# Kernel optimization log

Hardware: AMD Instinct MI355X
Metric: run time of the kernel (lower is better)

The kernel has to match this reference:

```python
import jax, jax.numpy as jnp
import numpy as np

N = 100000
E = 3200000
F_IN = 128
HID = 16
C = 8


def setup_inputs() -> dict:
    key = jax.random.key(0)
    k1, k2, k3, k4 = jax.random.split(key, 4)
    x = jax.random.normal(k1, (N, F_IN), dtype=jnp.float32)
    edge_index = jax.random.randint(k2, (2, E), 0, N, dtype=jnp.int64)
    W1 = jax.random.normal(k3, (F_IN, HID), dtype=jnp.float32) * (1.0 / np.sqrt(F_IN))
    b1 = jnp.zeros((HID,), dtype=jnp.float32)
    W2 = jax.random.normal(k4, (HID, C), dtype=jnp.float32) * (1.0 / np.sqrt(HID))
    b2 = jnp.zeros((C,), dtype=jnp.float32)
    return {"x": x, "edge_index": edge_index, "W1": W1, "b1": b1, "W2": W2, "b2": b2, "num_nodes": N}


def gcn_conv(x, src, dst, norm, W, b, num_nodes):
    # x: [N, F_in], src/dst: [E+N] (self-loops appended), norm: [E+N]
    h = x @ W                                # dense transform first (small out dim)
    msg = h[src] * norm[:, None]             # gather + edgewise scale
    out = jax.ops.segment_sum(msg, dst, num_segments=num_nodes)  # scatter-add
    return out + b


def reference(x, edge_index, W1, b1, W2, b2, num_nodes):
    # GCN normalization with self-loops: D^-1/2 (A+I) D^-1/2
    loop = jnp.arange(num_nodes, dtype=edge_index.dtype)
    src = jnp.concatenate([edge_index[0], loop])
    dst = jnp.concatenate([edge_index[1], loop])
    deg = jax.ops.segment_sum(jnp.ones_like(dst, dtype=x.dtype), dst, num_segments=num_nodes)
    dinv = jnp.where(deg > 0, jax.lax.rsqrt(deg), 0.0)
    norm = dinv[src] * dinv[dst]             # [E+N]

    h = jax.nn.relu(gcn_conv(x, src, dst, norm, W1, b1, num_nodes))
    # Dropout(p=0.5) in eval mode -> identity
    logits = gcn_conv(h, src, dst, norm, W2, b2, num_nodes)
    return jax.nn.log_softmax(logits, axis=1)
```

## Files before the change

### kernel.cpp

```cpp
#include <hip/hip_runtime.h>
#include <hip/hip_fp16.h>
#include <math.h>

#define FIN 128
#define HID 16
#define NC 8
#define BSH 8
#define BUKN 256
#define MAXBUK 512
#define CAP 10240
#define EPT 8
#define ACH (512 * EPT)

__device__ __forceinline__ __half2 shfl2(__half2 v, int m) {
    unsigned u = *(unsigned*)&v;
    u = __shfl_xor(u, m, 64);
    return *(__half2*)&u;
}

__global__ __launch_bounds__(512) void passA_kernel(
        const void* __restrict__ ei, int E, int N,
        int* __restrict__ pcur, unsigned* __restrict__ pakbuf, int nbuk) {
    const long long* p64 = (const long long*)ei;
    int ok = 1;
#pragma unroll
    for (int i = 0; i < 16; ++i) {
        long long v = p64[i];
        if (v < 0 || v >= (long long)N) ok = 0;
    }
    const int is64 = ok;
    const int* __restrict__ e32 = (const int*)ei;
    const int vecOK = is64 ? ((E & 1) == 0) : ((E & 3) == 0);
    __shared__ int cnt[MAXBUK], scn[MAXBUK], sbase[MAXBUK];
    __shared__ unsigned spv[ACH];
    __shared__ unsigned short sbk[ACH];
    const int t = threadIdx.x;
    for (long long c0 = (long long)blockIdx.x * ACH; c0 < E;
         c0 += (long long)gridDim.x * ACH) {
        cnt[t] = 0;
        __syncthreads();
        const long long e0 = c0 + (long long)t * EPT;
        const bool full = vecOK && (e0 + EPT <= E);
        int bv[EPT], rk[EPT];
        unsigned pv[EPT];
        if (full) {
            int ds[EPT], ss[EPT];
            if (is64) {
                const int4* pd = (const int4*)(e32 + 2 * ((long long)E + e0));
                const int4* ps = (const int4*)(e32 + 2 * e0);
                int4 a = pd[0], b = pd[1], c = pd[2], d = pd[3];
                ds[0]=a.x; ds[1]=a.z; ds[2]=b.x; ds[3]=b.z;
                ds[4]=c.x; ds[5]=c.z; ds[6]=d.x; ds[7]=d.z;
                int4 e = ps[0], f = ps[1], g = ps[2], h = ps[3];
                ss[0]=e.x; ss[1]=e.z; ss[2]=f.x; ss[3]=f.z;
                ss[4]=g.x; ss[5]=g.z; ss[6]=h.x; ss[7]=h.z;
            } else {
                const int4* pd = (const int4*)(e32 + (long long)E + e0);
                const int4* ps = (const int4*)(e32 + e0);
                int4 a = pd[0], b = pd[1];
                ds[0]=a.x; ds[1]=a.y; ds[2]=a.z; ds[3]=a.w;
                ds[4]=b.x; ds[5]=b.y; ds[6]=b.z; ds[7]=b.w;
                int4 e = ps[0], f = ps[1];
                ss[0]=e.x; ss[1]=e.y; ss[2]=e.z; ss[3]=e.w;
                ss[4]=f.x; ss[5]=f.y; ss[6]=f.z; ss[7]=f.w;
            }
#pragma unroll
            for (int i = 0; i < EPT; ++i) {
                int dd = ds[i];
                bv[i] = dd >> BSH;
                pv[i] = (unsigned)ss[i] | ((unsigned)(dd & (BUKN - 1)) << 24);
                rk[i] = atomicAdd(&cnt[bv[i]], 1);
            }
        } else {
#pragma unroll
            for (int i = 0; i < EPT; ++i) {
                long long e = e0 + i;
                bv[i] = -1;
                if (e < E) {
                    int dd = e32[is64 ? 2 * ((long long)E + e) : ((long long)E + e)];
                    int ssc = e32[is64 ? 2 * e : e];
                    bv[i] = dd >> BSH;
                    pv[i] = (unsigned)ssc | ((unsigned)(dd & (BUKN - 1)) << 24);
                    rk[i] = atomicAdd(&cnt[bv[i]], 1);
                }
            }
        }
        __syncthreads();
        int v = cnt[t];
        scn[t] = v;
        __syncthreads();
        for (int d = 1; d < MAXBUK; d <<= 1) {
            int add = (t >= d) ? scn[t - d] : 0;
            __syncthreads();
            scn[t] += add;
            __syncthreads();
        }
        int excl = scn[t] - v;
        __syncthreads();
        scn[t] = excl;
        if (t < nbuk) sbase[t] = v ? atomicAdd(&pcur[t * 16], v) : 0;
        __syncthreads();
#pragma unroll
        for (int i = 0; i < EPT; ++i) {
            if (bv[i] >= 0) {
                int s = scn[bv[i]] + rk[i];
                spv[s] = pv[i];
                sbk[s] = (unsigned short)bv[i];
            }
        }
        __syncthreads();
        int total = (int)((E - c0 < ACH) ? (E - c0) : ACH);
        for (int s = t; s < total; s += 512) {
            int b = sbk[s];
            int rel = sbase[b] + (s - scn[b]);
            if (rel < CAP) pakbuf[b * CAP + rel] = spv[s];
        }
        __syncthreads();
    }
}

__global__ __launch_bounds__(512) void passC2_kernel(
        const unsigned* __restrict__ pak, const int* __restrict__ pcur,
        int* __restrict__ csr_src, int* __restrict__ off,
        float* __restrict__ dinv, int N) {
    __shared__ int c[BUKN], sc[BUKN], cur[BUKN];
    const int b = blockIdx.x, t = threadIdx.x;
    if (t < BUKN) c[t] = 0;
    __syncthreads();
    const int ebeg = b * CAP;
    int cntb = pcur[b * 16];
    if (cntb > CAP) cntb = CAP;
    const int eend = ebeg + cntb;
    for (int i = ebeg + t; i < eend; i += 512)
        atomicAdd(&c[pak[i] >> 24], 1);
    __syncthreads();
    int v = (t < BUKN) ? c[t] : 0;
    if (t < BUKN) sc[t] = v;
    __syncthreads();
    for (int d = 1; d < 256; d <<= 1) {
        int add = (t < BUKN && t >= d) ? sc[t - d] : 0;
        __syncthreads();
        if (t < BUKN) sc[t] += add;
        __syncthreads();
    }
    if (t < BUKN) cur[t] = ebeg + sc[t] - v;
    __syncthreads();
    for (int i = ebeg + t; i < eend; i += 512) {
        unsigned w = pak[i];
        int pos = atomicAdd(&cur[w >> 24], 1);
        csr_src[pos] = (int)(w & 0xFFFFFFu);
    }
    __syncthreads();
    int n = (b << BSH) + t;
    if (t < BUKN && n < N) {
        off[n] = cur[t];
        dinv[n] = rsqrtf((float)(v + 1));
    }
}

__global__ void transform1_kernel(const float* __restrict__ x,
                                  const float* __restrict__ W1,
                                  const float* __restrict__ dinv,
                                  __half* __restrict__ g1, int N) {
    __shared__ float xs[16][FIN + 4];
    __shared__ float w[FIN][HID];
    const int t = threadIdx.x;
    for (int i = t; i < FIN * HID; i += 256) w[i / HID][i % HID] = W1[i];

    const float4* x4 = (const float4*)x;
    for (int rb = blockIdx.x * 16; rb < N; rb += gridDim.x * 16) {
        __syncthreads();
        for (int i = t; i < 16 * FIN / 4; i += 256) {
            int r = i >> 5, f4 = i & 31;
            int row = rb + r;
            float4 v = (row < N) ? x4[(size_t)row * (FIN / 4) + f4]
                                 : make_float4(0.f, 0.f, 0.f, 0.f);
            *((float4*)&xs[r][f4 * 4]) = v;
        }
        __syncthreads();
        int r = t >> 4, k = t & 15;
        int row = rb + r;
        if (row < N) {
            float s = 0.f;
#pragma unroll
            for (int f = 0; f < FIN; ++f) s += xs[r][f] * w[f][k];
            g1[(size_t)row * HID + k] = __float2half(s * dinv[row]);
        }
    }
}

__global__ void agg1_kernel(const int* __restrict__ off, const int* __restrict__ csr_src,
                            const __half2* __restrict__ g1h, const float* __restrict__ dinv,
                            const float* __restrict__ b1, const float* __restrict__ W2,
                            float4* __restrict__ g2q_out, int N) {
    const float4* g1q = (const float4*)g1h;
    __shared__ float w2s[HID][NC];
    for (int i = threadIdx.x; i < HID * NC; i += blockDim.x)
        w2s[i >> 3][i & 7] = W2[i];
    __syncthreads();
    int wid = threadIdx.x >> 6;
    int lane = threadIdx.x & 63;
    int sub = lane >> 4;
    int r = lane & 15;
    int hi = r & 1;
    int j = r >> 1;
    float4 bA = ((const float4*)b1)[hi * 2];
    float4 bB = ((const float4*)b1)[hi * 2 + 1];
    int wavesTotal = gridDim.x * (blockDim.x >> 6);
    for (int base = (blockIdx.x * (blockDim.x >> 6) + wid) * 4; base < N;
         base += wavesTotal * 4) {
        int n = base + sub;
        bool act = n < N;
        int start = 0, end = 0;
        float4 selfraw;
        if (act) {
            start = (n & (BUKN - 1)) ? off[n - 1] : (n >> BSH) * CAP;
            end = off[n];
            if (r < 2) selfraw = g1q[(size_t)n * 2 + hi];
        }
        __half2 a0 = __float2half2_rn(0.f), a1 = a0, a2 = a0, a3 = a0;
        for (int e = start + j; e < end; e += 8) {
            float4 raw = g1q[(size_t)csr_src[e] * 2 + hi];
            const __half2* rh = (const __half2*)&raw;
            a0 = __hadd2(a0, rh[0]); a1 = __hadd2(a1, rh[1]);
            a2 = __hadd2(a2, rh[2]); a3 = __hadd2(a3, rh[3]);
        }
#pragma unroll
        for (int m = 2; m <= 8; m <<= 1) {
            a0 = __hadd2(a0, shfl2(a0, m)); a1 = __hadd2(a1, shfl2(a1, m));
            a2 = __hadd2(a2, shfl2(a2, m)); a3 = __hadd2(a3, shfl2(a3, m));
        }
        if (act && r < 2) {
            float di = dinv[n];
            float2 s01 = __half22float2(a0), s23 = __half22float2(a1);
            float2 s45 = __half22float2(a2), s67 = __half22float2(a3);
            float2 f0 = __half22float2(*(__half2*)&selfraw.x);
            float2 f1 = __half22float2(*(__half2*)&selfraw.y);
            float2 f2 = __half22float2(*(__half2*)&selfraw.z);
            float2 f3 = __half22float2(*(__half2*)&selfraw.w);
            float h8[8];
            h8[0] = fmaxf(di * (s01.x + f0.x) + bA.x, 0.f);
            h8[1] = fmaxf(di * (s01.y + f0.y) + bA.y, 0.f);
            h8[2] = fmaxf(di * (s23.x + f1.x) + bA.z, 0.f);
            h8[3] = fmaxf(di * (s23.y + f1.y) + bA.w, 0.f);
            h8[4] = fmaxf(di * (s45.x + f2.x) + bB.x, 0.f);
            h8[5] = fmaxf(di * (s45.y + f2.y) + bB.y, 0.f);
            h8[6] = fmaxf(di * (s67.x + f3.x) + bB.z, 0.f);
            h8[7] = fmaxf(di * (s67.y + f3.y) + bB.w, 0.f);
            float part[8];
#pragma unroll
            for (int c = 0; c < 8; ++c) {
                float acc = 0.f;
#pragma unroll
                for (int k = 0; k < 8; ++k) acc += h8[k] * w2s[hi * 8 + k][c];
                part[c] = acc;
            }
#pragma unroll
            for (int c = 0; c < 8; ++c) part[c] += __shfl_xor(part[c], 1, 64);
            if (r == 0) {
                __half2 p0 = __floats2half2_rn(part[0] * di, part[1] * di);
                __half2 p1 = __floats2half2_rn(part[2] * di, part[3] * di);
                __half2 p2 = __floats2half2_rn(part[4] * di, part[5] * di);
                __half2 p3 = __floats2half2_rn(part[6] * di, part[7] * di);
                float4 o;
                *(__half2*)&o.x = p0; *(__half2*)&o.y = p1;
                *(__half2*)&o.z = p2; *(__half2*)&o.w = p3;
                g2q_out[n] = o;
            }
        }
    }
}

__global__ void agg2_kernel(const int* __restrict__ off, const int* __restrict__ csr_src,
                            const __half2* __restrict__ g2h, const float* __restrict__ dinv,
                            const float* __restrict__ b2, float* __restrict__ out, int N) {
    const float4* g2q = (const float4*)g2h;
    int wid = threadIdx.x >> 6;
    int lane = threadIdx.x & 63;
    int sub = lane >> 3, sl = lane & 7;
    float4 b2A = ((const float4*)b2)[0];
    float4 b2B = ((const float4*)b2)[1];
    int wavesTotal = gridDim.x * (blockDim.x >> 6);
    for (int base = (blockIdx.x * (blockDim.x >> 6) + wid) * 8; base < N;
         base += wavesTotal * 8) {
        int n = base + sub;
        bool act = n < N;
        int start = 0, end = 0;
        float4 selfraw;
        if (act) {
            start = (n & (BUKN - 1)) ? off[n - 1] : (n >> BSH) * CAP;
            end = off[n];
            selfraw = g2q[n];
        }
        __half2 a0 = __float2half2_rn(0.f), a1 = a0, a2 = a0, a3 = a0;
        for (int e = start + sl; e < end; e += 8) {
            float4 raw = g2q[csr_src[e]];
            const __half2* rh = (const __half2*)&raw;
            a0 = __hadd2(a0, rh[0]); a1 = __hadd2(a1, rh[1]);
            a2 = __hadd2(a2, rh[2]); a3 = __hadd2(a3, rh[3]);
        }
#pragma unroll
        for (int m = 1; m <= 4; m <<= 1) {
            a0 = __hadd2(a0, shfl2(a0, m)); a1 = __hadd2(a1, shfl2(a1, m));
            a2 = __hadd2(a2, shfl2(a2, m)); a3 = __hadd2(a3, shfl2(a3, m));
        }
        if (act) {
            float di = dinv[n];
            float2 s01 = __half22float2(a0), s23 = __half22float2(a1);
            float2 s45 = __half22float2(a2), s67 = __half22float2(a3);
            float2 f0 = __half22float2(*(__half2*)&selfraw.x);
            float2 f1 = __half22float2(*(__half2*)&selfraw.y);
            float2 f2 = __half22float2(*(__half2*)&selfraw.z);
            float2 f3 = __half22float2(*(__half2*)&selfraw.w);
            float l0 = di * (s01.x + f0.x) + b2A.x;
            float l1 = di * (s01.y + f0.y) + b2A.y;
            float l2 = di * (s23.x + f1.x) + b2A.z;
            float l3 = di * (s23.y + f1.y) + b2A.w;
            float l4 = di * (s45.x + f2.x) + b2B.x;
            float l5 = di * (s45.y + f2.y) + b2B.y;
            float l6 = di * (s67.x + f3.x) + b2B.z;
            float l7 = di * (s67.y + f3.y) + b2B.w;
            float m0 = fmaxf(fmaxf(fmaxf(l0, l1), fmaxf(l2, l3)),
                             fmaxf(fmaxf(l4, l5), fmaxf(l6, l7)));
            float se = __expf(l0 - m0) + __expf(l1 - m0) + __expf(l2 - m0) +
                       __expf(l3 - m0) + __expf(l4 - m0) + __expf(l5 - m0) +
                       __expf(l6 - m0) + __expf(l7 - m0);
            float lse = m0 + __logf(se);
            if (sl < 2) {
                float4 o;
                if (sl == 0) { o.x=l0-lse; o.y=l1-lse; o.z=l2-lse; o.w=l3-lse; }
                else         { o.x=l4-lse; o.y=l5-lse; o.z=l6-lse; o.w=l7-lse; }
                ((float4*)&out[(size_t)n * NC])[sl] = o;
            }
        }
    }
}

extern "C" void kernel_launch(void* const* d_in, const int* in_sizes, int n_in,
                              void* d_out, int out_size, void* d_ws, size_t ws_size,
                              hipStream_t stream) {
    const float* x  = (const float*)d_in[0];
    const void*  ei = d_in[1];
    const float* W1 = (const float*)d_in[2];
    const float* b1 = (const float*)d_in[3];
    const float* W2 = (const float*)d_in[4];
    const float* b2 = (const float*)d_in[5];

    const int N = in_sizes[0] / FIN;
    const int E = in_sizes[1] / 2;
    const int nbuk = (N + BUKN - 1) >> BSH;

    char* p = (char*)d_ws;
    unsigned* pakbuf = (unsigned*)p;     p += (size_t)nbuk * CAP * 4;
    int*    csr_src = (int*)p;           p += (size_t)nbuk * CAP * 4;
    __half* g1h     = (__half*)p;        p += (size_t)N * HID * 2;
    __half* g2h     = (__half*)p;        p += (size_t)N * NC * 2;
    int*    off     = (int*)p;           p += (size_t)N * 4;
    float*  dinv    = (float*)p;         p += (size_t)N * 4;
    int*    pcur    = (int*)p;           p += (size_t)MAXBUK * 16 * 4;

    hipMemsetAsync(pcur, 0, (size_t)MAXBUK * 16 * 4, stream);
    passA_kernel<<<(E + ACH - 1) / ACH, 512, 0, stream>>>(ei, E, N, pcur,
                                                          pakbuf, nbuk);
    passC2_kernel<<<nbuk, 512, 0, stream>>>(pakbuf, pcur, csr_src, off, dinv, N);

    int t1grid = (N + 15) / 16; if (t1grid > 2048) t1grid = 2048;
    transform1_kernel<<<t1grid, 256, 0, stream>>>(x, W1, dinv, g1h, N);
    agg1_kernel<<<(N + 15) / 16, 256, 0, stream>>>(off, csr_src, (const __half2*)g1h,
                                                   dinv, b1, W2, (float4*)g2h, N);
    agg2_kernel<<<(N + 31) / 32, 256, 0, stream>>>(off, csr_src, (const __half2*)g2h,
                                                   dinv, b2, (float*)d_out, N);
}
```

Measured before the change: 135.4 us.

## Stage bucket edges in LDS and unroll gather loops for more loads in flight

In the CSR build kernel, each bucket's packed edges are now copied into LDS during the counting pass and read back from LDS in the placement pass, so the second global read of the bucket is avoided. The two aggregation kernels now unroll the neighbour gather loop by two with separate accumulators, keeping two independent index/feature loads in flight per lane. The dense transform splits its dot product into four partial sums to break the serial FMA chain. The LDS staging adds 40KB of shared memory per block, which may reduce occupancy, and the extra accumulators raise register use.

After: 132.2 us. 1.02x faster.

```diff
diff --git a/kernel.cpp b/kernel.cpp
--- a/kernel.cpp
+++ b/kernel.cpp
@@ -124,15 +124,18 @@
         int* __restrict__ csr_src, int* __restrict__ off,
         float* __restrict__ dinv, int N) {
     __shared__ int c[BUKN], sc[BUKN], cur[BUKN];
+    __shared__ unsigned sld[CAP];
     const int b = blockIdx.x, t = threadIdx.x;
     if (t < BUKN) c[t] = 0;
     __syncthreads();
     const int ebeg = b * CAP;
     int cntb = pcur[b * 16];
     if (cntb > CAP) cntb = CAP;
-    const int eend = ebeg + cntb;
-    for (int i = ebeg + t; i < eend; i += 512)
-        atomicAdd(&c[pak[i] >> 24], 1);
+    for (int i = t; i < cntb; i += 512) {
+        unsigned w = pak[ebeg + i];
+        sld[i] = w;
+        atomicAdd(&c[w >> 24], 1);
+    }
     __syncthreads();
     int v = (t < BUKN) ? c[t] : 0;
     if (t < BUKN) sc[t] = v;
@@ -145,8 +148,8 @@
     }
     if (t < BUKN) cur[t] = ebeg + sc[t] - v;
     __syncthreads();
-    for (int i = ebeg + t; i < eend; i += 512) {
-        unsigned w = pak[i];
+    for (int i = t; i < cntb; i += 512) {
+        unsigned w = sld[i];
         int pos = atomicAdd(&cur[w >> 24], 1);
         csr_src[pos] = (int)(w & 0xFFFFFFu);
     }
@@ -181,10 +184,15 @@
         int r = t >> 4, k = t & 15;
         int row = rb + r;
         if (row < N) {
-            float s = 0.f;
-#pragma unroll
-            for (int f = 0; f < FIN; ++f) s += xs[r][f] * w[f][k];
-            g1[(size_t)row * HID + k] = __float2half(s * dinv[row]);
+            float s0 = 0.f, s1 = 0.f, s2 = 0.f, s3 = 0.f;
+#pragma unroll
+            for (int f = 0; f < FIN; f += 4) {
+                s0 += xs[r][f]     * w[f][k];
+                s1 += xs[r][f + 1] * w[f + 1][k];
+                s2 += xs[r][f + 2] * w[f + 2][k];
+                s3 += xs[r][f + 3] * w[f + 3][k];
+            }
+            g1[(size_t)row * HID + k] = __float2half(((s0 + s1) + (s2 + s3)) * dinv[row]);
         }
     }
 }
@@ -219,12 +227,27 @@
             if (r < 2) selfraw = g1q[(size_t)n * 2 + hi];
         }
         __half2 a0 = __float2half2_rn(0.f), a1 = a0, a2 = a0, a3 = a0;
-        for (int e = start + j; e < end; e += 8) {
-            float4 raw = g1q[(size_t)csr_src[e] * 2 + hi];
-            const __half2* rh = (const __half2*)&raw;
-            a0 = __hadd2(a0, rh[0]); a1 = __hadd2(a1, rh[1]);
-            a2 = __hadd2(a2, rh[2]); a3 = __hadd2(a3, rh[3]);
-        }
+        __half2 c0 = a0, c1 = a0, c2 = a0, c3 = a0;
+        int e = start + j;
+        for (; e + 8 < end; e += 16) {
+            int i0 = csr_src[e], i1 = csr_src[e + 8];
+            float4 r0 = g1q[(size_t)i0 * 2 + hi];
+            float4 r1 = g1q[(size_t)i1 * 2 + hi];
+            const __half2* h0 = (const __half2*)&r0;
+            const __half2* h1 = (const __half2*)&r1;
+            a0 = __hadd2(a0, h0[0]); a1 = __hadd2(a1, h0[1]);
+            a2 = __hadd2(a2, h0[2]); a3 = __hadd2(a3, h0[3]);
+            c0 = __hadd2(c0, h1[0]); c1 = __hadd2(c1, h1[1]);
+            c2 = __hadd2(c2, h1[2]); c3 = __hadd2(c3, h1[3]);
+        }
+        if (e < end) {
+            float4 r0 = g1q[(size_t)csr_src[e] * 2 + hi];
+            const __half2* h0 = (const __half2*)&r0;
+            a0 = __hadd2(a0, h0[0]); a1 = __hadd2(a1, h0[1]);
+            a2 = __hadd2(a2, h0[2]); a3 = __hadd2(a3, h0[3]);
+        }
+        a0 = __hadd2(a0, c0); a1 = __hadd2(a1, c1);
+        a2 = __hadd2(a2, c2); a3 = __hadd2(a3, c3);
 #pragma unroll
         for (int m = 2; m <= 8; m <<= 1) {
             a0 = __hadd2(a0, shfl2(a0, m)); a1 = __hadd2(a1, shfl2(a1, m));
@@ -293,12 +316,27 @@
             selfraw = g2q[n];
         }
         __half2 a0 = __float2half2_rn(0.f), a1 = a0, a2 = a0, a3 = a0;
-        for (int e = start + sl; e < end; e += 8) {
-            float4 raw = g2q[csr_src[e]];
-            const __half2* rh = (const __half2*)&raw;
-            a0 = __hadd2(a0, rh[0]); a1 = __hadd2(a1, rh[1]);
-            a2 = __hadd2(a2, rh[2]); a3 = __hadd2(a3, rh[3]);
-        }
+        __half2 c0 = a0, c1 = a0, c2 = a0, c3 = a0;
+        int e = start + sl;
+        for (; e + 8 < end; e += 16) {
+            int i0 = csr_src[e], i1 = csr_src[e + 8];
+            float4 r0 = g2q[i0];
+            float4 r1 = g2q[i1];
+            const __half2* h0 = (const __half2*)&r0;
+            const __half2* h1 = (const __half2*)&r1;
+            a0 = __hadd2(a0, h0[0]); a1 = __hadd2(a1, h0[1]);
+            a2 = __hadd2(a2, h0[2]); a3 = __hadd2(a3, h0[3]);
+            c0 = __hadd2(c0, h1[0]); c1 = __hadd2(c1, h1[1]);
+            c2 = __hadd2(c2, h1[2]); c3 = __hadd2(c3, h1[3]);
+        }
+        if (e < end) {
+            float4 r0 = g2q[csr_src[e]];
+            const __half2* h0 = (const __half2*)&r0;
+            a0 = __hadd2(a0, h0[0]); a1 = __hadd2(a1, h0[1]);
+            a2 = __hadd2(a2, h0[2]); a3 = __hadd2(a3, h0[3]);
+        }
+        a0 = __hadd2(a0, c0); a1 = __hadd2(a1, c1);
+        a2 = __hadd2(a2, c2); a3 = __hadd2(a3, c3);
 #pragma unroll
         for (int m = 1; m <= 4; m <<= 1) {
             a0 = __hadd2(a0, shfl2(a0, m)); a1 = __hadd2(a1, shfl2(a1, m));
```
